# Kernel tuning notes

Hardware: AMD Instinct MI355X
Metric: run time of the kernel (lower is better)

The kernel has to match this reference:

```python
import jax, jax.numpy as jnp
import numpy as np
from jax import lax

B, C, O, K, H, Wd = 8, 64, 64, 3, 128, 128


def setup_inputs() -> dict:
    key = jax.random.key(0)
    k1, k2, k3 = jax.random.split(key, 3)
    feat = jax.random.normal(k1, (B, C, H, Wd), dtype=jnp.float32)
    transform_mat = jax.random.normal(k2, (B, K * K, H * Wd), dtype=jnp.float32)
    # xavier-normal init for W [C, K, K, O]
    std = float(np.sqrt(2.0 / (C * K * K + O)))
    W = jax.random.normal(k3, (C, K, K, O), dtype=jnp.float32) * std
    return {"feat": feat, "transform_mat": transform_mat, "W": W}


def reference(feat, transform_mat, W):
    b, c, h, w = feat.shape
    L = h * w
    # unfold: [B, C*K*K, H, W] with channel-major (c, ki, kj) ordering, same as torch Unfold
    patches = lax.conv_general_dilated_patches(
        feat, filter_shape=(K, K), window_strides=(1, 1),
        padding=((1, 1), (1, 1)))
    p = patches.reshape(b, c, K * K, L)                 # [B, C, K*K, L]
    trans = jnp.transpose(transform_mat, (0, 2, 1))     # [B, L, K*K] (module's permute(0,2,1))
    Wr = W.reshape(c, K * K, -1)                        # [C, K*K, O]
    # dynamic weighted conv: per-location filter scales each patch tap before contraction
    out = jnp.einsum('bckl,blk,cko->bol', p, trans, Wr)  # [B, O, L]
    return out.reshape(b, -1, h, w)
```

## Files before the change

kernel.cpp:

```cpp
#include <hip/hip_runtime.h>

#define NTAP 9
#define C_DIM 64
#define O_DIM 64
#define HW 128
#define CPAD 72

typedef short s16x8 __attribute__((ext_vector_type(8)));
typedef float f32x16 __attribute__((ext_vector_type(16)));

__device__ __forceinline__ unsigned short f2bf(float x) {
    unsigned int u = __float_as_uint(x);
    unsigned int r = (u + 0x7fffu + ((u >> 16) & 1u)) >> 16;
    return (unsigned short)r;
}

__global__ void swizzle_W_kernel(const float* __restrict__ W,
                                 unsigned short* __restrict__ Wf) {
    int idx = blockIdx.x * 256 + threadIdx.x;
    if (idx >= NTAP * 4 * 2 * 64 * 8) return;
    int e    = idx & 7;
    int lane = (idx >> 3) & 63;
    int m    = (idx >> 9) & 1;
    int s    = (idx >> 10) & 3;
    int tap  = idx >> 12;
    int c = s * 16 + ((lane >> 5) << 3) + e;
    int o = (m << 5) + (lane & 31);
    Wf[idx] = f2bf(W[c * 576 + tap * 64 + o]);
}

__global__ __launch_bounds__(256, 5) void dyconv_kernel(
    const float* __restrict__ feat, const float* __restrict__ tm,
    const unsigned short* __restrict__ Wf, float* __restrict__ out)
{
    __shared__ __align__(16) unsigned short feat_lds[10][18][CPAD];

    const int flat  = blockIdx.x;
    const int b     = flat & 7;
    const int inner = flat >> 3;
    const int h0    = (inner >> 3) * 8;
    const int w0    = (inner & 7) * 16;

    const int tid = threadIdx.x;

    for (int T = tid; T < 320; T += 256) {
        const int r    = T >> 5;
        const int rem  = T & 31;
        const int wg   = rem & 3;
        const int coct = rem >> 2;
        const int hr   = h0 - 1 + r;
        const bool inb = (hr >= 0) && (hr < HW);
        const float* src = feat + (((size_t)(b * C_DIM + coct * 8)) * HW + hr) * HW
                         + w0 + wg * 4;
        float4 v[8];
        #pragma unroll
        for (int j = 0; j < 8; ++j)
            v[j] = inb ? *(const float4*)(src + (size_t)j * (HW * HW))
                       : float4{0.f, 0.f, 0.f, 0.f};
        #pragma unroll
        for (int i = 0; i < 4; ++i) {
            s16x8 pk;
            #pragma unroll
            for (int j = 0; j < 8; ++j) {
                const float* vf = (const float*)&v[j];
                pk[j] = (short)f2bf(vf[i]);
            }
            *(s16x8*)&feat_lds[r][wg * 4 + i + 1][coct * 8] = pk;
        }
    }
    for (int i = tid; i < 1280; i += 256) {
        const int r    = i >> 7;
        const int rem  = i & 127;
        const int c    = rem & 63;
        const int side = rem >> 6;
        const int hr   = h0 - 1 + r;
        const int gw   = w0 + (side ? 16 : -1);
        float v = 0.f;
        if (hr >= 0 && hr < HW && gw >= 0 && gw < HW)
            v = feat[(((size_t)(b * C_DIM + c)) * HW + hr) * HW + gw];
        feat_lds[r][side ? 17 : 0][c] = f2bf(v);
    }

    const int lane = tid & 63;
    const int wave = tid >> 6;
    const int g    = lane >> 5;
    const int c31  = lane & 31;
    const int prow = c31 >> 4;
    const int pw   = c31 & 15;
    const int hout = h0 + wave * 2 + prow;
    const int wout = w0 + pw;
    const int lrow = wave * 2 + prow;

    __syncthreads();

    const s16x8* __restrict__ Wf8 = (const s16x8*)Wf;

    f32x16 acc0 = {0,0,0,0,0,0,0,0,0,0,0,0,0,0,0,0};
    f32x16 acc1 = acc0;

    #pragma unroll
    for (int tap = 0; tap < NTAP; ++tap) {
        const int di = tap / 3;
        const int dj = tap % 3;
        const s16x8* bp = (const s16x8*)&feat_lds[lrow + di][pw + dj][0];
        const float tv = tm[((size_t)(b * NTAP + tap)) * (HW * HW)
                            + (size_t)hout * HW + wout];
        f32x16 pa = {0,0,0,0,0,0,0,0,0,0,0,0,0,0,0,0};
        f32x16 pb = pa;
        #pragma unroll
        for (int s = 0; s < 4; ++s) {
            s16x8 bf = bp[2 * s + g];
            s16x8 a0 = Wf8[((tap * 4 + s) * 2 + 0) * 64 + lane];
            s16x8 a1 = Wf8[((tap * 4 + s) * 2 + 1) * 64 + lane];
            pa = __builtin_amdgcn_mfma_f32_32x32x16_bf16(a0, bf, pa, 0, 0, 0);
            pb = __builtin_amdgcn_mfma_f32_32x32x16_bf16(a1, bf, pb, 0, 0, 0);
        }
        #pragma unroll
        for (int r = 0; r < 16; ++r) {
            acc0[r] = fmaf(tv, pa[r], acc0[r]);
            acc1[r] = fmaf(tv, pb[r], acc1[r]);
        }
    }

    float* op = out + ((size_t)b * O_DIM) * (HW * HW) + (size_t)hout * HW + wout;
    #pragma unroll
    for (int r = 0; r < 16; ++r) {
        const int o = (r & 3) + ((r >> 2) << 3) + (g << 2);
        op[(size_t)o        * (HW * HW)] = acc0[r];
        op[(size_t)(o + 32) * (HW * HW)] = acc1[r];
    }
}

extern "C" void kernel_launch(void* const* d_in, const int* in_sizes, int n_in,
                              void* d_out, int out_size, void* d_ws, size_t ws_size,
                              hipStream_t stream) {
    const float* feat = (const float*)d_in[0];
    const float* tm   = (const float*)d_in[1];
    const float* W    = (const float*)d_in[2];
    float* out        = (float*)d_out;
    unsigned short* Wf = (unsigned short*)d_ws;

    swizzle_W_kernel<<<dim3(144), dim3(256), 0, stream>>>(W, Wf);
    dyconv_kernel<<<dim3(1024), dim3(256), 0, stream>>>(feat, tm, Wf, out);
}
```

Before: 35.27 us.

## Process two width tiles per block with double-buffered LDS staging

Each block now covers two adjacent 16-wide output tiles, halving the grid to 512 blocks. The second tile's feature halo is loaded into a second LDS buffer while the first tile's MFMAs run. The halo columns now come in as float4 loads instead of scalar loads, and the transform values are prefetched into registers. s_setprio is raised around the MFMA loop. In exchange, LDS per block doubles and occupancy drops (launch bound 5 to 4), and with 512 blocks there may be too few waves to fill the GPU.

Result: slower. 43.16 us (+22.4%).

```diff
diff --git a/kernel.cpp b/kernel.cpp
--- a/kernel.cpp
+++ b/kernel.cpp
@@ -29,57 +29,50 @@
     Wf[idx] = f2bf(W[c * 576 + tap * 64 + o]);
 }
 
-__global__ __launch_bounds__(256, 5) void dyconv_kernel(
+__global__ __launch_bounds__(256, 4) void dyconv_kernel(
     const float* __restrict__ feat, const float* __restrict__ tm,
     const unsigned short* __restrict__ Wf, float* __restrict__ out)
 {
-    __shared__ __align__(16) unsigned short feat_lds[10][18][CPAD];
+    __shared__ __align__(16) unsigned short feat_lds[2][10][18][CPAD];
 
     const int flat  = blockIdx.x;
     const int b     = flat & 7;
     const int inner = flat >> 3;
-    const int h0    = (inner >> 3) * 8;
-    const int w0    = (inner & 7) * 16;
+    const int h0    = (inner >> 2) * 8;
+    const int w0p   = (inner & 3) * 32;
 
     const int tid = threadIdx.x;
 
-    for (int T = tid; T < 320; T += 256) {
-        const int r    = T >> 5;
-        const int rem  = T & 31;
-        const int wg   = rem & 3;
-        const int coct = rem >> 2;
-        const int hr   = h0 - 1 + r;
-        const bool inb = (hr >= 0) && (hr < HW);
-        const float* src = feat + (((size_t)(b * C_DIM + coct * 8)) * HW + hr) * HW
-                         + w0 + wg * 4;
-        float4 v[8];
-        #pragma unroll
-        for (int j = 0; j < 8; ++j)
-            v[j] = inb ? *(const float4*)(src + (size_t)j * (HW * HW))
-                       : float4{0.f, 0.f, 0.f, 0.f};
-        #pragma unroll
-        for (int i = 0; i < 4; ++i) {
-            s16x8 pk;
+    auto stage = [&](int buf, int w0) {
+        for (int U = tid; U < 480; U += 256) {
+            const int r    = U / 48;
+            const int rem  = U % 48;
+            const int q    = rem % 6;
+            const int c0   = (rem / 6) * 8;
+            const int hr   = h0 - 1 + r;
+            const int wb   = w0 - 4 + 4 * q;
+            const bool ld  = (hr >= 0) && (hr < HW) && (wb >= 0) && (wb <= HW - 4);
+            const float* src = feat + (((size_t)(b * C_DIM + c0)) * HW + hr) * HW + wb;
+            float4 v[8];
             #pragma unroll
-            for (int j = 0; j < 8; ++j) {
-                const float* vf = (const float*)&v[j];
-                pk[j] = (short)f2bf(vf[i]);
+            for (int j = 0; j < 8; ++j)
+                v[j] = ld ? *(const float4*)(src + (size_t)j * (HW * HW))
+                          : float4{0.f, 0.f, 0.f, 0.f};
+            #pragma unroll
+            for (int i = 0; i < 4; ++i) {
+                const int wi = 4 * q - 3 + i;
+                if (wi >= 0 && wi <= 17) {
+                    s16x8 pk;
+                    #pragma unroll
+                    for (int j = 0; j < 8; ++j) {
+                        const float* vf = (const float*)&v[j];
+                        pk[j] = (short)f2bf(vf[i]);
+                    }
+                    *(s16x8*)&feat_lds[buf][r][wi][c0] = pk;
+                }
             }
-            *(s16x8*)&feat_lds[r][wg * 4 + i + 1][coct * 8] = pk;
         }
-    }
-    for (int i = tid; i < 1280; i += 256) {
-        const int r    = i >> 7;
-        const int rem  = i & 127;
-        const int c    = rem & 63;
-        const int side = rem >> 6;
-        const int hr   = h0 - 1 + r;
-        const int gw   = w0 + (side ? 16 : -1);
-        float v = 0.f;
-        if (hr >= 0 && hr < HW && gw >= 0 && gw < HW)
-            v = feat[(((size_t)(b * C_DIM + c)) * HW + hr) * HW + gw];
-        feat_lds[r][side ? 17 : 0][c] = f2bf(v);
-    }
+    };
 
     const int lane = tid & 63;
     const int wave = tid >> 6;
@@ -88,46 +81,64 @@
     const int prow = c31 >> 4;
     const int pw   = c31 & 15;
     const int hout = h0 + wave * 2 + prow;
-    const int wout = w0 + pw;
     const int lrow = wave * 2 + prow;
-
-    __syncthreads();
 
     const s16x8* __restrict__ Wf8 = (const s16x8*)Wf;
 
-    f32x16 acc0 = {0,0,0,0,0,0,0,0,0,0,0,0,0,0,0,0};
-    f32x16 acc1 = acc0;
+    stage(0, w0p);
+    __syncthreads();
 
     #pragma unroll
-    for (int tap = 0; tap < NTAP; ++tap) {
-        const int di = tap / 3;
-        const int dj = tap % 3;
-        const s16x8* bp = (const s16x8*)&feat_lds[lrow + di][pw + dj][0];
-        const float tv = tm[((size_t)(b * NTAP + tap)) * (HW * HW)
-                            + (size_t)hout * HW + wout];
-        f32x16 pa = {0,0,0,0,0,0,0,0,0,0,0,0,0,0,0,0};
-        f32x16 pb = pa;
+    for (int pp = 0; pp < 2; ++pp) {
+        const int w0   = w0p + pp * 16;
+        const int wout = w0 + pw;
+
+        float tmr[NTAP];
         #pragma unroll
-        for (int s = 0; s < 4; ++s) {
-            s16x8 bf = bp[2 * s + g];
-            s16x8 a0 = Wf8[((tap * 4 + s) * 2 + 0) * 64 + lane];
-            s16x8 a1 = Wf8[((tap * 4 + s) * 2 + 1) * 64 + lane];
-            pa = __builtin_amdgcn_mfma_f32_32x32x16_bf16(a0, bf, pa, 0, 0, 0);
-            pb = __builtin_amdgcn_mfma_f32_32x32x16_bf16(a1, bf, pb, 0, 0, 0);
+        for (int t = 0; t < NTAP; ++t)
+            tmr[t] = tm[((size_t)(b * NTAP + t)) * (HW * HW)
+                        + (size_t)hout * HW + wout];
+
+        if (pp == 0) stage(1, w0p + 16);
+
+        f32x16 acc0 = {0,0,0,0,0,0,0,0,0,0,0,0,0,0,0,0};
+        f32x16 acc1 = acc0;
+
+        __builtin_amdgcn_s_setprio(1);
+        #pragma unroll
+        for (int tap = 0; tap < NTAP; ++tap) {
+            const int di = tap / 3;
+            const int dj = tap % 3;
+            const s16x8* bp = (const s16x8*)&feat_lds[pp][lrow + di][pw + dj][0];
+            f32x16 pa = {0,0,0,0,0,0,0,0,0,0,0,0,0,0,0,0};
+            f32x16 pb = pa;
+            #pragma unroll
+            for (int s = 0; s < 4; ++s) {
+                s16x8 bf = bp[2 * s + g];
+                s16x8 a0 = Wf8[((tap * 4 + s) * 2 + 0) * 64 + lane];
+                s16x8 a1 = Wf8[((tap * 4 + s) * 2 + 1) * 64 + lane];
+                pa = __builtin_amdgcn_mfma_f32_32x32x16_bf16(a0, bf, pa, 0, 0, 0);
+                pb = __builtin_amdgcn_mfma_f32_32x32x16_bf16(a1, bf, pb, 0, 0, 0);
+            }
+            const float tv = tmr[tap];
+            #pragma unroll
+            for (int r = 0; r < 16; ++r) {
+                acc0[r] = fmaf(tv, pa[r], acc0[r]);
+                acc1[r] = fmaf(tv, pb[r], acc1[r]);
+            }
         }
+        __builtin_amdgcn_s_setprio(0);
+
+        float* op = out + ((size_t)b * O_DIM) * (HW * HW)
+                  + (size_t)hout * HW + wout;
         #pragma unroll
         for (int r = 0; r < 16; ++r) {
-            acc0[r] = fmaf(tv, pa[r], acc0[r]);
-            acc1[r] = fmaf(tv, pb[r], acc1[r]);
+            const int o = (r & 3) + ((r >> 2) << 3) + (g << 2);
+            op[(size_t)o        * (HW * HW)] = acc0[r];
+            op[(size_t)(o + 32) * (HW * HW)] = acc1[r];
         }
-    }
 
-    float* op = out + ((size_t)b * O_DIM) * (HW * HW) + (size_t)hout * HW + wout;
-    #pragma unroll
-    for (int r = 0; r < 16; ++r) {
-        const int o = (r & 3) + ((r >> 2) << 3) + (g << 2);
-        op[(size_t)o        * (HW * HW)] = acc0[r];
-        op[(size_t)(o + 32) * (HW * HW)] = acc1[r];
+        if (pp == 0) __syncthreads();
     }
 }
 
@@ -141,5 +152,5 @@
     unsigned short* Wf = (unsigned short*)d_ws;
 
     swizzle_W_kernel<<<dim3(144), dim3(256), 0, stream>>>(W, Wf);
-    dyconv_kernel<<<dim3(1024), dim3(256), 0, stream>>>(feat, tm, Wf, out);
+    dyconv_kernel<<<dim3(512), dim3(256), 0, stream>>>(feat, tm, Wf, out);
 }
```
